# Performance work log

Measured on AMD Instinct MI355X. Metric: run time of the kernel, lower is better.

The kernel has to match this reference:

```python
import jax, jax.numpy as jnp
import numpy as np

N, F_IN, F_OUT = 8192, 512, 256
ALPHA = 0.2  # LeakyReLU negative slope
MASK_FILL = 9e-15  # value used by the original for non-edges (NOT -inf)


def setup_inputs() -> dict:
    key = jax.random.key(0)
    k1, k2, k3, k4 = jax.random.split(key, 4)
    x = jax.random.normal(k1, (N, F_IN), dtype=jnp.float32)
    adj = jax.random.randint(k2, (N, N), 0, 2, dtype=jnp.int32)
    # xavier_uniform-like scale
    wscale = np.sqrt(2.0) * np.sqrt(6.0 / (F_IN + F_OUT))
    ascale = np.sqrt(2.0) * np.sqrt(6.0 / (2 * F_OUT + 1))
    W = jax.random.uniform(k3, (F_IN, F_OUT), jnp.float32, -wscale, wscale)
    a = jax.random.uniform(k4, (2 * F_OUT, 1), jnp.float32, -ascale, ascale)
    return {"x": x, "adj": adj, "W": W, "a": a}


def reference(x, adj, W, a):
    # h: [N, F_OUT]
    h = x @ W
    # score_ij = leakyrelu(cat(h_i, h_j) . a) = leakyrelu(h_i.a1 + h_j.a2)
    a1 = a[:F_OUT, 0]   # [F_OUT]
    a2 = a[F_OUT:, 0]   # [F_OUT]
    f1 = h @ a1         # [N]
    f2 = h @ a2         # [N]
    e = jax.nn.leaky_relu(f1[:, None] + f2[None, :], negative_slope=ALPHA)  # [N, N]
    att = jnp.where(adj > 0, e, jnp.float32(MASK_FILL))
    att = jax.nn.softmax(att, axis=1)
    # dropout is a no-op (p=0.0 / inference)
    h_prime = att @ h   # [N, F_OUT]
    return h_prime
```

## Files before the change

kernel.cpp:

```cpp
#include <hip/hip_runtime.h>
#include <hip/hip_bf16.h>
#include <stdint.h>

#define NN 8192
#define FIN 512
#define FOUT 256
#define ALPHAV 0.2f
#define MASKF 9e-15f
#define L2E 1.44269504088896340736f

typedef __attribute__((ext_vector_type(8))) short bf16x8;
typedef __attribute__((ext_vector_type(16))) float f32x16;

static __device__ __forceinline__ float ex2(float x){
#if __has_builtin(__builtin_amdgcn_exp2f)
  return __builtin_amdgcn_exp2f(x);
#else
  return exp2f(x);
#endif
}
static __device__ __forceinline__ unsigned short f2bf(float f){
  __bf16 b = (__bf16)f;
  return __builtin_bit_cast(unsigned short, b);
}
static __device__ __forceinline__ float bf2f(unsigned short u){
  unsigned int v = ((unsigned int)u) << 16;
  return __builtin_bit_cast(float, v);
}

__global__ __launch_bounds__(256) void k_prep(
    const float* __restrict__ Wm, unsigned short* __restrict__ WtHi,
    unsigned short* __restrict__ WtLo)
{
  __shared__ float ls[16 * 256];
  const int t = threadIdx.x;
  const int S = blockIdx.x;
  const int k0 = S * 16;
  {
    const int kk = t >> 4;
    const int n0 = (t & 15) * 16;
#pragma unroll
    for (int q = 0; q < 4; ++q) {
      float4 v = *(const float4*)(Wm + (size_t)(k0 + kk) * FOUT + n0 + q * 4);
      *(float4*)(&ls[kk * 256 + n0 + q * 4]) = v;
    }
  }
  __syncthreads();
  float v[16];
  unsigned short hh[16], ll[16];
#pragma unroll
  for (int kk = 0; kk < 16; ++kk) {
    v[kk] = ls[kk * 256 + t];
    hh[kk] = f2bf(v[kk]);
    ll[kk] = f2bf(v[kk] - bf2f(hh[kk]));
  }
  unsigned short* oh = WtHi + (size_t)S * 4096 + t * 8;
  unsigned short* ol = WtLo + (size_t)S * 4096 + t * 8;
#pragma unroll
  for (int g = 0; g < 2; ++g) {
    ushort4 a, b, c, d;
    a.x = hh[g*8+0]; a.y = hh[g*8+1]; a.z = hh[g*8+2]; a.w = hh[g*8+3];
    b.x = hh[g*8+4]; b.y = hh[g*8+5]; b.z = hh[g*8+6]; b.w = hh[g*8+7];
    c.x = ll[g*8+0]; c.y = ll[g*8+1]; c.z = ll[g*8+2]; c.w = ll[g*8+3];
    d.x = ll[g*8+4]; d.y = ll[g*8+5]; d.z = ll[g*8+6]; d.w = ll[g*8+7];
    *(ushort4*)(oh + g * 2048)     = a;
    *(ushort4*)(oh + g * 2048 + 4) = b;
    *(ushort4*)(ol + g * 2048)     = c;
    *(ushort4*)(ol + g * 2048 + 4) = d;
  }
}

__global__ __launch_bounds__(256, 1) void k_gemm_h(
    const float* __restrict__ x, const unsigned short* __restrict__ WtHi,
    const unsigned short* __restrict__ WtLo, const float* __restrict__ aG,
    unsigned short* __restrict__ hTt, float* __restrict__ f1,
    float* __restrict__ f2)
{
  __shared__ __align__(16) unsigned short xhi[16384];
  __shared__ __align__(16) unsigned short xlo[16384];
  __shared__ __align__(16) unsigned short wsh[3][4096];
  __shared__ __align__(16) unsigned short wsl[3][4096];
  __shared__ __align__(16) float as2[512];
  __shared__ float f1red[4][32], f2red[4][32];

  const int t  = threadIdx.x;
  const int wv = t >> 6;
  const int l  = t & 63;
  const int lh = l >> 5;
  const int lm = l & 31;
  const int i0 = blockIdx.x * 32;

  if (t < 128) {
    float4 v = *(const float4*)(aG + t * 4);
    *(float4*)(&as2[t * 4]) = v;
  }
  {
    const int xi = t >> 3;
    const int kb = (t & 7) * 4;
    const float* xrow = x + (size_t)(i0 + xi) * FIN;
    const int kgb = (t & 7) >> 1;
    const int bo  = (t & 1) * 4;
#pragma unroll
    for (int q = 0; q < 16; ++q) {
      float4 v = *(const float4*)(xrow + kb + q * 32);
      ushort4 h4, l4;
      h4.x = f2bf(v.x); l4.x = f2bf(v.x - bf2f(h4.x));
      h4.y = f2bf(v.y); l4.y = f2bf(v.y - bf2f(h4.y));
      h4.z = f2bf(v.z); l4.z = f2bf(v.z - bf2f(h4.z));
      h4.w = f2bf(v.w); l4.w = f2bf(v.w - bf2f(h4.w));
      const int idx = (q * 4 + kgb) * 256 + xi * 8 + bo;
      *(ushort4*)(&xhi[idx]) = h4;
      *(ushort4*)(&xlo[idx]) = l4;
    }
  }

  f32x16 acc0, acc1;
#pragma unroll
  for (int e = 0; e < 16; ++e) { acc0[e] = 0.f; acc1[e] = 0.f; }

#define SB0 __builtin_amdgcn_sched_barrier(0)
#define WSTAGE(B, S)                                                          \
  do {                                                                        \
    const unsigned short* gh_ = WtHi + (size_t)(S) * 4096 + t * 8;            \
    const unsigned short* gl_ = WtLo + (size_t)(S) * 4096 + t * 8;            \
    __builtin_amdgcn_global_load_lds(                                         \
        (const __attribute__((address_space(1))) unsigned int*)gh_,           \
        (__attribute__((address_space(3))) unsigned int*)(&wsh[B][t * 8]), 16, 0, 0); \
    __builtin_amdgcn_global_load_lds(                                         \
        (const __attribute__((address_space(1))) unsigned int*)(gh_ + 2048),  \
        (__attribute__((address_space(3))) unsigned int*)(&wsh[B][2048 + t * 8]), 16, 0, 0); \
    __builtin_amdgcn_global_load_lds(                                         \
        (const __attribute__((address_space(1))) unsigned int*)gl_,           \
        (__attribute__((address_space(3))) unsigned int*)(&wsl[B][t * 8]), 16, 0, 0); \
    __builtin_amdgcn_global_load_lds(                                         \
        (const __attribute__((address_space(1))) unsigned int*)(gl_ + 2048),  \
        (__attribute__((address_space(3))) unsigned int*)(&wsl[B][2048 + t * 8]), 16, 0, 0); \
  } while (0)

#define GTS(S, BUF, DOISSUE, NBUF, VMC)                                       \
  do {                                                                        \
    asm volatile("s_waitcnt vmcnt(" #VMC ")" ::: "memory");                   \
    __builtin_amdgcn_s_barrier();                                             \
    SB0;                                                                      \
    if (DOISSUE) WSTAGE(NBUF, (S) + 2);                                       \
    SB0;                                                                      \
    const int kgb_ = ((S) * 2 + lh) * 512 + lm * 16;                          \
    bf16x8 bh_ = *(const bf16x8*)(((const char*)xhi) + kgb_);                 \
    bf16x8 bl_ = *(const bf16x8*)(((const char*)xlo) + kgb_);                 \
    const int na_ = lh * 4096 + (wv * 64 + lm) * 16;                          \
    bf16x8 ah0_ = *(const bf16x8*)(((const char*)&wsh[BUF][0]) + na_);        \
    bf16x8 al0_ = *(const bf16x8*)(((const char*)&wsl[BUF][0]) + na_);        \
    bf16x8 ah1_ = *(const bf16x8*)(((const char*)&wsh[BUF][0]) + na_ + 512);  \
    bf16x8 al1_ = *(const bf16x8*)(((const char*)&wsl[BUF][0]) + na_ + 512);  \
    acc0 = __builtin_amdgcn_mfma_f32_32x32x16_bf16(ah0_, bh_, acc0, 0, 0, 0); \
    acc1 = __builtin_amdgcn_mfma_f32_32x32x16_bf16(ah1_, bh_, acc1, 0, 0, 0); \
    acc0 = __builtin_amdgcn_mfma_f32_32x32x16_bf16(ah0_, bl_, acc0, 0, 0, 0); \
    acc1 = __builtin_amdgcn_mfma_f32_32x32x16_bf16(ah1_, bl_, acc1, 0, 0, 0); \
    acc0 = __builtin_amdgcn_mfma_f32_32x32x16_bf16(al0_, bh_, acc0, 0, 0, 0); \
    acc1 = __builtin_amdgcn_mfma_f32_32x32x16_bf16(al1_, bh_, acc1, 0, 0, 0); \
  } while (0)

  asm volatile("s_waitcnt vmcnt(0)" ::: "memory");
  SB0;
  WSTAGE(0, 0);
  SB0;
  WSTAGE(1, 1);
  asm volatile("s_waitcnt lgkmcnt(0)" ::: "memory");
  SB0;

#pragma unroll 1
  for (int p = 0; p < 10; ++p) {
    const int s0 = p * 3;
    GTS(s0 + 0, 0, 1, 2, 4);
    GTS(s0 + 1, 1, 1, 0, 4);
    GTS(s0 + 2, 2, 1, 1, 4);
  }
  GTS(30, 0, 0, 2, 4);
  GTS(31, 1, 0, 0, 0);
#undef SB0
#undef WSTAGE
#undef GTS

  float p1 = 0.f, p2 = 0.f;
#pragma unroll
  for (int reg = 0; reg < 16; ++reg) {
    const int nl = (reg & 3) + 8 * (reg >> 2) + 4 * lh;
    p1 += acc0[reg] * as2[wv * 64 + nl]       + acc1[reg] * as2[wv * 64 + 32 + nl];
    p2 += acc0[reg] * as2[256 + wv * 64 + nl] + acc1[reg] * as2[256 + wv * 64 + 32 + nl];
  }
  p1 += __shfl_xor(p1, 32);
  p2 += __shfl_xor(p2, 32);
  if (l < 32) { f1red[wv][l] = p1; f2red[wv][l] = p2; }
  __syncthreads();
  if (t < 32) {
    f1[i0 + t] = f1red[0][t] + f1red[1][t] + f1red[2][t] + f1red[3][t];
    f2[i0 + t] = f2red[0][t] + f2red[1][t] + f2red[2][t] + f2red[3][t];
  }

  const size_t hb = (size_t)(i0 >> 5) * 8192 + (size_t)(lm >> 3) * 2048 + (lm & 7);
#pragma unroll
  for (int reg = 0; reg < 16; ++reg) {
    const int nl = (reg & 3) + 8 * (reg >> 2) + 4 * lh;
    hTt[hb + (size_t)(wv * 64 + nl) * 8]      = f2bf(acc0[reg]);
    hTt[hb + (size_t)(wv * 64 + 32 + nl) * 8] = f2bf(acc1[reg]);
  }
}

__global__ __launch_bounds__(1024) void k_bound(
    const float* __restrict__ f1, const float* __restrict__ f2,
    float* __restrict__ mhat)
{
  __shared__ float red[16];
  const int t = threadIdx.x;
  float m = -3.0e38f;
#pragma unroll
  for (int k = 0; k < 8; ++k) m = fmaxf(m, f2[t + k * 1024]);
#pragma unroll
  for (int off = 32; off > 0; off >>= 1) m = fmaxf(m, __shfl_xor(m, off));
  if ((t & 63) == 0) red[t >> 6] = m;
  __syncthreads();
  float fm = red[0];
#pragma unroll
  for (int w = 1; w < 16; ++w) fm = fmaxf(fm, red[w]);
#pragma unroll
  for (int k = 0; k < 8; ++k) {
    int i = t + k * 1024;
    float s = f1[i] + fm;
    mhat[i] = fmaxf(fmaxf(s, ALPHAV * s), MASKF);
  }
}

__global__ __launch_bounds__(256, 2) void k_spmm(
    const unsigned short* __restrict__ hTt,
    const int* __restrict__ adj,
    const float* __restrict__ f1, const float* __restrict__ f2,
    const float* __restrict__ mhat,
    float* __restrict__ part, float* __restrict__ rowsumP)
{
  __shared__ __align__(16) unsigned short hbuf[3 * 8192];
  __shared__ __align__(16) unsigned int mskL[32 * 129];
  __shared__ __align__(16) float f2s[1024];
  const int t  = threadIdx.x;
  const int wv = t >> 6;
  const int l  = t & 63;
  const int lh = l >> 5;
  const int lm = l & 31;
  const int bx = blockIdx.x;
  const int ks = blockIdx.y;
  const int r0 = bx * 128;
  const int lh8 = lh * 8;

  const int rA = r0 + wv * 32 + lm;
  const float nmA   = -mhat[rA] * L2E;
  const float base0 = fmaf(f1[rA], L2E, nmA);
  const float c20   = nmA * (1.f - ALPHAV);
  const float mc0   = fmaf(MASKF, L2E, nmA);

  {
    float4 v = *(const float4*)(f2 + ks * 1024 + t * 4);
    v.x *= L2E; v.y *= L2E; v.z *= L2E; v.w *= L2E;
    *(float4*)(&f2s[t * 4]) = v;
  }

  {
    const int jt = t & 31;
    const int r8 = t >> 5;
    const int* gp = adj + (size_t)(r0 + r8) * NN + ks * 1024 + jt * 32;
#pragma unroll 2
    for (int p = 0; p < 16; ++p) {
      const int* rp = gp + (size_t)p * 8 * NN;
      int4 v[8];
#pragma unroll
      for (int c = 0; c < 8; ++c) v[c] = *(const int4*)(rp + c * 4);
      unsigned int m = 0;
#pragma unroll
      for (int c = 0; c < 8; ++c) {
        m |= (v[c].x > 0 ? 1u : 0u) << (c * 4 + 0);
        m |= (v[c].y > 0 ? 1u : 0u) << (c * 4 + 1);
        m |= (v[c].z > 0 ? 1u : 0u) << (c * 4 + 2);
        m |= (v[c].w > 0 ? 1u : 0u) << (c * 4 + 3);
      }
      mskL[jt * 129 + p * 8 + r8] = m;
    }
  }
  __builtin_amdgcn_sched_barrier(0);

  f32x16 acc[8];
#pragma unroll
  for (int c = 0; c < 8; ++c)
#pragma unroll
    for (int e = 0; e < 16; ++e) acc[c][e] = 0.f;
  float sumP = 0.f;

  const unsigned short* gt0 = hTt + (size_t)ks * 32 * 8192;
  const char* cbase = (const char*)hbuf;
  const int mrow = wv * 32 + lm;

#define SB0 __builtin_amdgcn_sched_barrier(0)
#define STAGE(BUFI, JT)                                                       \
  do {                                                                        \
    const unsigned short* gp_ = gt0 + (size_t)(JT) * 8192 + t * 8;            \
    char* lp_ = ((char*)hbuf) + (BUFI) * 16384 + t * 16;                      \
    _Pragma("unroll")                                                         \
    for (int c = 0; c < 4; ++c) {                                             \
      __builtin_amdgcn_global_load_lds(                                       \
          (const __attribute__((address_space(1))) unsigned int*)(gp_ + c * 2048), \
          (__attribute__((address_space(3))) unsigned int*)(lp_ + c * 4096),  \
          16, 0, 0);                                                          \
    }                                                                         \
  } while (0)

#define REGEN8(AFR, MB, FB)                                                   \
  do {                                                                        \
    float4 fx_ = *(const float4*)(&f2s[FB]);                                  \
    float4 fy_ = *(const float4*)(&f2s[(FB) + 4]);                            \
    float fv_[8] = {fx_.x, fx_.y, fx_.z, fx_.w, fy_.x, fy_.y, fy_.z, fy_.w};  \
    _Pragma("unroll")                                                         \
    for (int b = 0; b < 8; ++b) {                                             \
      float u_ = base0 + fv_[b];                                              \
      float w_ = fmaxf(u_, fmaf(ALPHAV, u_, c20));                            \
      w_ = (((MB) >> b) & 1u) ? w_ : mc0;                                     \
      float p_ = ex2(w_);                                                     \
      sumP += p_;                                                             \
      AFR[b] = (short)f2bf(p_);                                               \
    }                                                                         \
  } while (0)

#define TS(JT, BUF, NBUF, DOISSUE, VMC)                                       \
  do {                                                                        \
    asm volatile("s_waitcnt vmcnt(" #VMC ")" ::: "memory");                   \
    __builtin_amdgcn_s_barrier();                                             \
    SB0;                                                                      \
    if (DOISSUE) STAGE(NBUF, (JT) + 2);                                       \
    SB0;                                                                      \
    const unsigned int m_ = mskL[(JT) * 129 + mrow];                          \
    bf16x8 afr0_, afr1_;                                                      \
    REGEN8(afr0_, m_ >> lh8,        (JT) * 32 + lh8);                         \
    REGEN8(afr1_, m_ >> (16 + lh8), (JT) * 32 + 16 + lh8);                    \
    SB0;                                                                      \
    const char* lb_ = cbase + (BUF) * 16384;                                  \
    const int g0_ = lh * 4096;                                                \
    const int g1_ = (2 + lh) * 4096;                                          \
    const int cb_ = lm * 16;                                                  \
    _Pragma("unroll")                                                         \
    for (int c = 0; c < 8; ++c) {                                             \
      bf16x8 b0_ = *(const bf16x8*)(lb_ + g0_ + c * 512 + cb_);               \
      acc[c] = __builtin_amdgcn_mfma_f32_32x32x16_bf16(afr0_, b0_, acc[c], 0, 0, 0); \
      bf16x8 b1_ = *(const bf16x8*)(lb_ + g1_ + c * 512 + cb_);               \
      acc[c] = __builtin_amdgcn_mfma_f32_32x32x16_bf16(afr1_, b1_, acc[c], 0, 0, 0); \
    }                                                                         \
  } while (0)

  STAGE(0, 0);
  SB0;
  STAGE(1, 1);
  asm volatile("s_waitcnt lgkmcnt(0)" ::: "memory");
  SB0;

#pragma unroll 1
  for (int p = 0; p < 10; ++p) {
    const int s0 = p * 3;
    TS(s0 + 0, 0, 2, 1, 4);
    TS(s0 + 1, 1, 0, 1, 4);
    TS(s0 + 2, 2, 1, 1, 4);
  }
  TS(30, 0, 2, 0, 4);
  TS(31, 1, 0, 0, 0);

#undef SB0
#undef STAGE
#undef REGEN8
#undef TS

  sumP += __shfl_xor(sumP, 32);
  if (lh == 0) rowsumP[(size_t)ks * NN + rA] = sumP;

  float* dst = part + (size_t)ks * NN * FOUT;
  const int rowb = r0 + wv * 32 + 4 * lh;
#pragma unroll
  for (int c = 0; c < 8; ++c) {
    const int col = c * 32 + lm;
#pragma unroll
    for (int reg = 0; reg < 16; ++reg) {
      int row = rowb + (reg & 3) + 8 * (reg >> 2);
      dst[(size_t)row * FOUT + col] = acc[c][reg];
    }
  }
}

__global__ __launch_bounds__(256) void k_fin(
    float* __restrict__ outp, const float* __restrict__ part,
    const float* __restrict__ rowsumP)
{
  const int idx4 = blockIdx.x * 256 + threadIdx.x;
  const size_t e = (size_t)idx4 * 4;
  const int i = (int)(e >> 8);
  float rs = 0.f;
#pragma unroll
  for (int p = 0; p < 8; ++p) rs += rowsumP[(size_t)p * NN + i];
  float4 o = {0.f, 0.f, 0.f, 0.f};
#pragma unroll
  for (int p = 0; p < 8; ++p) {
    float4 pv = *(const float4*)(part + (size_t)p * NN * FOUT + e);
    o.x += pv.x; o.y += pv.y; o.z += pv.z; o.w += pv.w;
  }
  float inv = 1.f / rs;
  o.x *= inv; o.y *= inv; o.z *= inv; o.w *= inv;
  *(float4*)(outp + e) = o;
}

extern "C" void kernel_launch(void* const* d_in, const int* in_sizes, int n_in,
                              void* d_out, int out_size, void* d_ws, size_t ws_size,
                              hipStream_t stream)
{
  const float* x  = (const float*)d_in[0];
  const int* adj  = (const int*)d_in[1];
  const float* Wm = (const float*)d_in[2];
  const float* aG = (const float*)d_in[3];
  float* outp = (float*)d_out;

  char* w = (char*)d_ws;
  unsigned short* hTt  = (unsigned short*)(w + 0);
  float* f1            = (float*)(w + 4194304);
  float* f2            = (float*)(w + 4227072);
  float* mhat          = (float*)(w + 4259840);
  float* rowsumP       = (float*)(w + 4292608);
  unsigned short* WtHi = (unsigned short*)(w + 4554752);
  unsigned short* WtLo = (unsigned short*)(w + 4816896);
  float* part          = (float*)(w + 5079040);

  hipLaunchKernelGGL(k_prep,   dim3(32),    dim3(256),  0, stream, Wm, WtHi, WtLo);
  hipLaunchKernelGGL(k_gemm_h, dim3(256),   dim3(256),  0, stream, x, WtHi, WtLo, aG, hTt, f1, f2);
  hipLaunchKernelGGL(k_bound,  dim3(1),     dim3(1024), 0, stream, f1, f2, mhat);
  hipLaunchKernelGGL(k_spmm,   dim3(64, 8), dim3(256),  0, stream, hTt, adj, f1, f2, mhat, part, rowsumP);
  hipLaunchKernelGGL(k_fin,    dim3(2048),  dim3(256),  0, stream, outp, part, rowsumP);
}
```

Baseline: 137.8 us.

## Stream adjacency mask loads through the main loop instead of a prologue

```diff
diff --git a/kernel.cpp b/kernel.cpp
--- a/kernel.cpp
+++ b/kernel.cpp
@@ -238,7 +238,7 @@
     float* __restrict__ part, float* __restrict__ rowsumP)
 {
   __shared__ __align__(16) unsigned short hbuf[3 * 8192];
-  __shared__ __align__(16) unsigned int mskL[32 * 129];
+  __shared__ __align__(16) unsigned int mskR[4][128];
   __shared__ __align__(16) float f2s[1024];
   const int t  = threadIdx.x;
   const int wv = t >> 6;
@@ -256,50 +256,42 @@
   const float c20   = nmA * (1.f - ALPHAV);
   const float mc0   = fmaf(MASKF, L2E, nmA);
 
+  const int* aQ = adj + (size_t)(r0 + (t >> 1)) * NN + ks * 1024 + (t & 1) * 16;
+
   {
     float4 v = *(const float4*)(f2 + ks * 1024 + t * 4);
     v.x *= L2E; v.y *= L2E; v.z *= L2E; v.w *= L2E;
     *(float4*)(&f2s[t * 4]) = v;
   }
 
-  {
-    const int jt = t & 31;
-    const int r8 = t >> 5;
-    const int* gp = adj + (size_t)(r0 + r8) * NN + ks * 1024 + jt * 32;
-#pragma unroll 2
-    for (int p = 0; p < 16; ++p) {
-      const int* rp = gp + (size_t)p * 8 * NN;
-      int4 v[8];
-#pragma unroll
-      for (int c = 0; c < 8; ++c) v[c] = *(const int4*)(rp + c * 4);
-      unsigned int m = 0;
-#pragma unroll
-      for (int c = 0; c < 8; ++c) {
-        m |= (v[c].x > 0 ? 1u : 0u) << (c * 4 + 0);
-        m |= (v[c].y > 0 ? 1u : 0u) << (c * 4 + 1);
-        m |= (v[c].z > 0 ? 1u : 0u) << (c * 4 + 2);
-        m |= (v[c].w > 0 ? 1u : 0u) << (c * 4 + 3);
-      }
-      mskL[jt * 129 + p * 8 + r8] = m;
-    }
-  }
-  __builtin_amdgcn_sched_barrier(0);
-
-  f32x16 acc[8];
-#pragma unroll
-  for (int c = 0; c < 8; ++c)
-#pragma unroll
-    for (int e = 0; e < 16; ++e) acc[c][e] = 0.f;
-  float sumP = 0.f;
-
-  const unsigned short* gt0 = hTt + (size_t)ks * 32 * 8192;
-  const char* cbase = (const char*)hbuf;
-  const int mrow = wv * 32 + lm;
-
 #define SB0 __builtin_amdgcn_sched_barrier(0)
+#define CONV(R0, R1, R2, R3, SLOT)                                            \
+  do {                                                                        \
+    unsigned int mb_ = 0;                                                     \
+    mb_ |= (R0.x > 0 ? 1u : 0u) << 0;  mb_ |= (R0.y > 0 ? 1u : 0u) << 1;      \
+    mb_ |= (R0.z > 0 ? 1u : 0u) << 2;  mb_ |= (R0.w > 0 ? 1u : 0u) << 3;      \
+    mb_ |= (R1.x > 0 ? 1u : 0u) << 4;  mb_ |= (R1.y > 0 ? 1u : 0u) << 5;      \
+    mb_ |= (R1.z > 0 ? 1u : 0u) << 6;  mb_ |= (R1.w > 0 ? 1u : 0u) << 7;      \
+    mb_ |= (R2.x > 0 ? 1u : 0u) << 8;  mb_ |= (R2.y > 0 ? 1u : 0u) << 9;      \
+    mb_ |= (R2.z > 0 ? 1u : 0u) << 10; mb_ |= (R2.w > 0 ? 1u : 0u) << 11;     \
+    mb_ |= (R3.x > 0 ? 1u : 0u) << 12; mb_ |= (R3.y > 0 ? 1u : 0u) << 13;     \
+    mb_ |= (R3.z > 0 ? 1u : 0u) << 14; mb_ |= (R3.w > 0 ? 1u : 0u) << 15;     \
+    unsigned int ob_ = __shfl_xor(mb_, 1);                                    \
+    if (!(t & 1)) mskR[SLOT][t >> 1] = mb_ | (ob_ << 16);                     \
+  } while (0)
+
+#define ADJR(R0, R1, R2, R3, W)                                               \
+  do {                                                                        \
+    R0 = *(const int4*)(aQ + (W) * 32);                                       \
+    R1 = *(const int4*)(aQ + (W) * 32 + 4);                                   \
+    R2 = *(const int4*)(aQ + (W) * 32 + 8);                                   \
+    R3 = *(const int4*)(aQ + (W) * 32 + 12);                                  \
+  } while (0)
+
 #define STAGE(BUFI, JT)                                                       \
   do {                                                                        \
-    const unsigned short* gp_ = gt0 + (size_t)(JT) * 8192 + t * 8;            \
+    const unsigned short* gp_ = hTt + (size_t)ks * 32 * 8192                  \
+                                + (size_t)(JT) * 8192 + t * 8;                \
     char* lp_ = ((char*)hbuf) + (BUFI) * 16384 + t * 16;                      \
     _Pragma("unroll")                                                         \
     for (int c = 0; c < 4; ++c) {                                             \
@@ -326,14 +318,16 @@
     }                                                                         \
   } while (0)
 
-#define TS(JT, BUF, NBUF, DOISSUE, VMC)                                       \
+#define TS(JT, BUF, NBUF, R0, R1, R2, R3, DOCONV, DOSTAGE, DOADJ, VMC)        \
   do {                                                                        \
     asm volatile("s_waitcnt vmcnt(" #VMC ")" ::: "memory");                   \
     __builtin_amdgcn_s_barrier();                                             \
     SB0;                                                                      \
-    if (DOISSUE) STAGE(NBUF, (JT) + 2);                                       \
+    if (DOCONV) CONV(R0, R1, R2, R3, ((JT) + 2) & 3);                         \
+    if (DOSTAGE) STAGE(NBUF, (JT) + 2);                                       \
+    if (DOADJ) ADJR(R0, R1, R2, R3, (JT) + 4);                                \
     SB0;                                                                      \
-    const unsigned int m_ = mskL[(JT) * 129 + mrow];                          \
+    const unsigned int m_ = mskR[(JT) & 3][mrow];                             \
     bf16x8 afr0_, afr1_;                                                      \
     REGEN8(afr0_, m_ >> lh8,        (JT) * 32 + lh8);                         \
     REGEN8(afr1_, m_ >> (16 + lh8), (JT) * 32 + 16 + lh8);                    \
@@ -351,23 +345,58 @@
     }                                                                         \
   } while (0)
 
+  {
+    int4 a0 = *(const int4*)(aQ + 0),  a1 = *(const int4*)(aQ + 4);
+    int4 a2 = *(const int4*)(aQ + 8),  a3 = *(const int4*)(aQ + 12);
+    CONV(a0, a1, a2, a3, 0);
+    int4 b0 = *(const int4*)(aQ + 32), b1 = *(const int4*)(aQ + 36);
+    int4 b2 = *(const int4*)(aQ + 40), b3 = *(const int4*)(aQ + 44);
+    CONV(b0, b1, b2, b3, 1);
+  }
+  SB0;
+
+  f32x16 acc[8];
+#pragma unroll
+  for (int c = 0; c < 8; ++c)
+#pragma unroll
+    for (int e = 0; e < 16; ++e) acc[c][e] = 0.f;
+  float sumP = 0.f;
+
+  const char* cbase = (const char*)hbuf;
+  const int mrow = wv * 32 + lm;
+
+  int4 X0, X1, X2, X3, Y0, Y1, Y2, Y3;
+
   STAGE(0, 0);
+  ADJR(X0, X1, X2, X3, 2);
   SB0;
   STAGE(1, 1);
+  ADJR(Y0, Y1, Y2, Y3, 3);
   asm volatile("s_waitcnt lgkmcnt(0)" ::: "memory");
   SB0;
 
 #pragma unroll 1
-  for (int p = 0; p < 10; ++p) {
-    const int s0 = p * 3;
-    TS(s0 + 0, 0, 2, 1, 4);
-    TS(s0 + 1, 1, 0, 1, 4);
-    TS(s0 + 2, 2, 1, 1, 4);
-  }
-  TS(30, 0, 2, 0, 4);
-  TS(31, 1, 0, 0, 0);
+  for (int p = 0; p < 4; ++p) {
+    const int s0 = p * 6;
+    TS(s0 + 0, 0, 2, X0, X1, X2, X3, 1, 1, 1, 8);
+    TS(s0 + 1, 1, 0, Y0, Y1, Y2, Y3, 1, 1, 1, 8);
+    TS(s0 + 2, 2, 1, X0, X1, X2, X3, 1, 1, 1, 8);
+    TS(s0 + 3, 0, 2, Y0, Y1, Y2, Y3, 1, 1, 1, 8);
+    TS(s0 + 4, 1, 0, X0, X1, X2, X3, 1, 1, 1, 8);
+    TS(s0 + 5, 2, 1, Y0, Y1, Y2, Y3, 1, 1, 1, 8);
+  }
+  TS(24, 0, 2, X0, X1, X2, X3, 1, 1, 1, 8);
+  TS(25, 1, 0, Y0, Y1, Y2, Y3, 1, 1, 1, 8);
+  TS(26, 2, 1, X0, X1, X2, X3, 1, 1, 1, 8);
+  TS(27, 0, 2, Y0, Y1, Y2, Y3, 1, 1, 1, 8);
+  TS(28, 1, 0, X0, X1, X2, X3, 1, 1, 0, 8);
+  TS(29, 2, 1, Y0, Y1, Y2, Y3, 1, 1, 0, 4);
+  TS(30, 0, 2, X0, X1, X2, X3, 0, 0, 0, 4);
+  TS(31, 1, 0, Y0, Y1, Y2, Y3, 0, 0, 0, 0);
 
 #undef SB0
+#undef CONV
+#undef ADJR
 #undef STAGE
 #undef REGEN8
 #undef TS
```

Result: slower. 174.5 us (+26.6%).

## Halve spmm row tile, split waves 2x2 over columns, and prefetch next attention fragment

Applied to the files above, without the earlier changes.

```diff
diff --git a/kernel.cpp b/kernel.cpp
--- a/kernel.cpp
+++ b/kernel.cpp
@@ -238,19 +238,21 @@
     float* __restrict__ part, float* __restrict__ rowsumP)
 {
   __shared__ __align__(16) unsigned short hbuf[3 * 8192];
-  __shared__ __align__(16) unsigned int mskL[32 * 129];
+  __shared__ __align__(16) unsigned int mskL[32 * 66];
   __shared__ __align__(16) float f2s[1024];
   const int t  = threadIdx.x;
   const int wv = t >> 6;
   const int l  = t & 63;
   const int lh = l >> 5;
   const int lm = l & 31;
+  const int wr = wv >> 1;
+  const int wc = wv & 1;
   const int bx = blockIdx.x;
   const int ks = blockIdx.y;
-  const int r0 = bx * 128;
+  const int r0 = bx * 64;
   const int lh8 = lh * 8;
 
-  const int rA = r0 + wv * 32 + lm;
+  const int rA = r0 + wr * 32 + lm;
   const float nmA   = -mhat[rA] * L2E;
   const float base0 = fmaf(f1[rA], L2E, nmA);
   const float c20   = nmA * (1.f - ALPHAV);
@@ -267,7 +269,7 @@
     const int r8 = t >> 5;
     const int* gp = adj + (size_t)(r0 + r8) * NN + ks * 1024 + jt * 32;
 #pragma unroll 2
-    for (int p = 0; p < 16; ++p) {
+    for (int p = 0; p < 8; ++p) {
       const int* rp = gp + (size_t)p * 8 * NN;
       int4 v[8];
 #pragma unroll
@@ -280,26 +282,28 @@
         m |= (v[c].z > 0 ? 1u : 0u) << (c * 4 + 2);
         m |= (v[c].w > 0 ? 1u : 0u) << (c * 4 + 3);
       }
-      mskL[jt * 129 + p * 8 + r8] = m;
+      mskL[jt * 66 + p * 8 + r8] = m;
     }
   }
+  asm volatile("s_waitcnt lgkmcnt(0)" ::: "memory");
+  __builtin_amdgcn_s_barrier();
   __builtin_amdgcn_sched_barrier(0);
 
-  f32x16 acc[8];
-#pragma unroll
-  for (int c = 0; c < 8; ++c)
+  f32x16 acc[4];
+#pragma unroll
+  for (int c = 0; c < 4; ++c)
 #pragma unroll
     for (int e = 0; e < 16; ++e) acc[c][e] = 0.f;
   float sumP = 0.f;
 
-  const unsigned short* gt0 = hTt + (size_t)ks * 32 * 8192;
   const char* cbase = (const char*)hbuf;
-  const int mrow = wv * 32 + lm;
+  const int mrow = wr * 32 + lm;
 
 #define SB0 __builtin_amdgcn_sched_barrier(0)
 #define STAGE(BUFI, JT)                                                       \
   do {                                                                        \
-    const unsigned short* gp_ = gt0 + (size_t)(JT) * 8192 + t * 8;            \
+    const unsigned short* gp_ = hTt + (size_t)ks * 32 * 8192                  \
+                                + (size_t)(JT) * 8192 + t * 8;                \
     char* lp_ = ((char*)hbuf) + (BUFI) * 16384 + t * 16;                      \
     _Pragma("unroll")                                                         \
     for (int c = 0; c < 4; ++c) {                                             \
@@ -326,60 +330,69 @@
     }                                                                         \
   } while (0)
 
-#define TS(JT, BUF, NBUF, DOISSUE, VMC)                                       \
+#define REGEN_STEP(A0, A1, JT)                                                \
+  do {                                                                        \
+    const unsigned int m_ = mskL[(JT) * 66 + mrow];                           \
+    REGEN8(A0, m_ >> lh8,        (JT) * 32 + lh8);                            \
+    REGEN8(A1, m_ >> (16 + lh8), (JT) * 32 + 16 + lh8);                       \
+  } while (0)
+
+#define TS(JT, BUF, NBUF, C0, C1, N0, N1, DOREGEN, DOSTAGE, VMC)              \
   do {                                                                        \
     asm volatile("s_waitcnt vmcnt(" #VMC ")" ::: "memory");                   \
     __builtin_amdgcn_s_barrier();                                             \
     SB0;                                                                      \
-    if (DOISSUE) STAGE(NBUF, (JT) + 2);                                       \
+    if (DOSTAGE) STAGE(NBUF, (JT) + 2);                                       \
     SB0;                                                                      \
-    const unsigned int m_ = mskL[(JT) * 129 + mrow];                          \
-    bf16x8 afr0_, afr1_;                                                      \
-    REGEN8(afr0_, m_ >> lh8,        (JT) * 32 + lh8);                         \
-    REGEN8(afr1_, m_ >> (16 + lh8), (JT) * 32 + 16 + lh8);                    \
-    SB0;                                                                      \
+    if (DOREGEN) REGEN_STEP(N0, N1, (JT) + 1);                                \
     const char* lb_ = cbase + (BUF) * 16384;                                  \
     const int g0_ = lh * 4096;                                                \
     const int g1_ = (2 + lh) * 4096;                                          \
-    const int cb_ = lm * 16;                                                  \
+    const int cb_ = (wc * 128 + lm) * 16;                                     \
     _Pragma("unroll")                                                         \
-    for (int c = 0; c < 8; ++c) {                                             \
+    for (int c = 0; c < 4; ++c) {                                             \
       bf16x8 b0_ = *(const bf16x8*)(lb_ + g0_ + c * 512 + cb_);               \
-      acc[c] = __builtin_amdgcn_mfma_f32_32x32x16_bf16(afr0_, b0_, acc[c], 0, 0, 0); \
+      acc[c] = __builtin_amdgcn_mfma_f32_32x32x16_bf16(C0, b0_, acc[c], 0, 0, 0); \
       bf16x8 b1_ = *(const bf16x8*)(lb_ + g1_ + c * 512 + cb_);               \
-      acc[c] = __builtin_amdgcn_mfma_f32_32x32x16_bf16(afr1_, b1_, acc[c], 0, 0, 0); \
+      acc[c] = __builtin_amdgcn_mfma_f32_32x32x16_bf16(C1, b1_, acc[c], 0, 0, 0); \
     }                                                                         \
   } while (0)
 
+  bf16x8 aE0, aE1, aO0, aO1;
+  REGEN_STEP(aE0, aE1, 0);
+  SB0;
   STAGE(0, 0);
   SB0;
   STAGE(1, 1);
-  asm volatile("s_waitcnt lgkmcnt(0)" ::: "memory");
   SB0;
 
 #pragma unroll 1
-  for (int p = 0; p < 10; ++p) {
-    const int s0 = p * 3;
-    TS(s0 + 0, 0, 2, 1, 4);
-    TS(s0 + 1, 1, 0, 1, 4);
-    TS(s0 + 2, 2, 1, 1, 4);
-  }
-  TS(30, 0, 2, 0, 4);
-  TS(31, 1, 0, 0, 0);
+  for (int p = 0; p < 5; ++p) {
+    const int s0 = p * 6;
+    TS(s0 + 0, 0, 2, aE0, aE1, aO0, aO1, 1, 1, 4);
+    TS(s0 + 1, 1, 0, aO0, aO1, aE0, aE1, 1, 1, 4);
+    TS(s0 + 2, 2, 1, aE0, aE1, aO0, aO1, 1, 1, 4);
+    TS(s0 + 3, 0, 2, aO0, aO1, aE0, aE1, 1, 1, 4);
+    TS(s0 + 4, 1, 0, aE0, aE1, aO0, aO1, 1, 1, 4);
+    TS(s0 + 5, 2, 1, aO0, aO1, aE0, aE1, 1, 1, 4);
+  }
+  TS(30, 0, 2, aE0, aE1, aO0, aO1, 1, 0, 4);
+  TS(31, 1, 0, aO0, aO1, aE0, aE1, 0, 0, 0);
 
 #undef SB0
 #undef STAGE
 #undef REGEN8
+#undef REGEN_STEP
 #undef TS
 
   sumP += __shfl_xor(sumP, 32);
-  if (lh == 0) rowsumP[(size_t)ks * NN + rA] = sumP;
+  if (lh == 0 && wc == 0) rowsumP[(size_t)ks * NN + rA] = sumP;
 
   float* dst = part + (size_t)ks * NN * FOUT;
-  const int rowb = r0 + wv * 32 + 4 * lh;
-#pragma unroll
-  for (int c = 0; c < 8; ++c) {
-    const int col = c * 32 + lm;
+  const int rowb = r0 + wr * 32 + 4 * lh;
+#pragma unroll
+  for (int c = 0; c < 4; ++c) {
+    const int col = wc * 128 + c * 32 + lm;
 #pragma unroll
     for (int reg = 0; reg < 16; ++reg) {
       int row = rowb + (reg & 3) + 8 * (reg >> 2);
@@ -429,9 +442,9 @@
   unsigned short* WtLo = (unsigned short*)(w + 4816896);
   float* part          = (float*)(w + 5079040);
 
-  hipLaunchKernelGGL(k_prep,   dim3(32),    dim3(256),  0, stream, Wm, WtHi, WtLo);
-  hipLaunchKernelGGL(k_gemm_h, dim3(256),   dim3(256),  0, stream, x, WtHi, WtLo, aG, hTt, f1, f2);
-  hipLaunchKernelGGL(k_bound,  dim3(1),     dim3(1024), 0, stream, f1, f2, mhat);
-  hipLaunchKernelGGL(k_spmm,   dim3(64, 8), dim3(256),  0, stream, hTt, adj, f1, f2, mhat, part, rowsumP);
-  hipLaunchKernelGGL(k_fin,    dim3(2048),  dim3(256),  0, stream, outp, part, rowsumP);
-}
+  hipLaunchKernelGGL(k_prep,   dim3(32),     dim3(256),  0, stream, Wm, WtHi, WtLo);
+  hipLaunchKernelGGL(k_gemm_h, dim3(256),    dim3(256),  0, stream, x, WtHi, WtLo, aG, hTt, f1, f2);
+  hipLaunchKernelGGL(k_bound,  dim3(1),      dim3(1024), 0, stream, f1, f2, mhat);
+  hipLaunchKernelGGL(k_spmm,   dim3(128, 8), dim3(256),  0, stream, hTt, adj, f1, f2, mhat, part, rowsumP);
+  hipLaunchKernelGGL(k_fin,    dim3(2048),   dim3(256),  0, stream, outp, part, rowsumP);
+}
```

New measurement: 151.2 us. 9.7% more time.

## Stream adjacency mask loads into MFMA loop and store bf16 partials

Applied to the files above, without the earlier changes.

```diff
diff --git a/kernel.cpp b/kernel.cpp
--- a/kernel.cpp
+++ b/kernel.cpp
@@ -235,10 +235,10 @@
     const int* __restrict__ adj,
     const float* __restrict__ f1, const float* __restrict__ f2,
     const float* __restrict__ mhat,
-    float* __restrict__ part, float* __restrict__ rowsumP)
+    unsigned short* __restrict__ partB, float* __restrict__ rowsumP)
 {
   __shared__ __align__(16) unsigned short hbuf[3 * 8192];
-  __shared__ __align__(16) unsigned int mskL[32 * 129];
+  __shared__ __align__(16) unsigned int mskD[2][8][128];
   __shared__ __align__(16) float f2s[1024];
   const int t  = threadIdx.x;
   const int wv = t >> 6;
@@ -249,6 +249,8 @@
   const int ks = blockIdx.y;
   const int r0 = bx * 128;
   const int lh8 = lh * 8;
+  const int arow = t >> 3;
+  const int awrd = t & 7;
 
   const int rA = r0 + wv * 32 + lm;
   const float nmA   = -mhat[rA] * L2E;
@@ -262,44 +264,45 @@
     *(float4*)(&f2s[t * 4]) = v;
   }
 
-  {
-    const int jt = t & 31;
-    const int r8 = t >> 5;
-    const int* gp = adj + (size_t)(r0 + r8) * NN + ks * 1024 + jt * 32;
-#pragma unroll 2
-    for (int p = 0; p < 16; ++p) {
-      const int* rp = gp + (size_t)p * 8 * NN;
-      int4 v[8];
-#pragma unroll
-      for (int c = 0; c < 8; ++c) v[c] = *(const int4*)(rp + c * 4);
-      unsigned int m = 0;
-#pragma unroll
-      for (int c = 0; c < 8; ++c) {
-        m |= (v[c].x > 0 ? 1u : 0u) << (c * 4 + 0);
-        m |= (v[c].y > 0 ? 1u : 0u) << (c * 4 + 1);
-        m |= (v[c].z > 0 ? 1u : 0u) << (c * 4 + 2);
-        m |= (v[c].w > 0 ? 1u : 0u) << (c * 4 + 3);
-      }
-      mskL[jt * 129 + p * 8 + r8] = m;
-    }
-  }
-  __builtin_amdgcn_sched_barrier(0);
-
-  f32x16 acc[8];
-#pragma unroll
-  for (int c = 0; c < 8; ++c)
-#pragma unroll
-    for (int e = 0; e < 16; ++e) acc[c][e] = 0.f;
-  float sumP = 0.f;
-
-  const unsigned short* gt0 = hTt + (size_t)ks * 32 * 8192;
-  const char* cbase = (const char*)hbuf;
-  const int mrow = wv * 32 + lm;
+  int4 g0, g1, g2, g3, g4, g5, g6, g7;
 
 #define SB0 __builtin_amdgcn_sched_barrier(0)
+#define ADJP(P, CN)                                                           \
+  do {                                                                        \
+    const int* ap_ = adj + (size_t)(r0 + (P) * 32 + arow) * NN                \
+                     + ks * 1024 + (CN) * 256 + awrd * 32;                    \
+    g0 = ((const int4*)ap_)[0]; g1 = ((const int4*)ap_)[1];                   \
+    g2 = ((const int4*)ap_)[2]; g3 = ((const int4*)ap_)[3];                   \
+    g4 = ((const int4*)ap_)[4]; g5 = ((const int4*)ap_)[5];                   \
+    g6 = ((const int4*)ap_)[6]; g7 = ((const int4*)ap_)[7];                   \
+  } while (0)
+
+#define CONVP(P, PAR)                                                         \
+  do {                                                                        \
+    unsigned int m_ = 0;                                                      \
+    m_ |= (g0.x>0?1u:0u)<<0;  m_ |= (g0.y>0?1u:0u)<<1;                        \
+    m_ |= (g0.z>0?1u:0u)<<2;  m_ |= (g0.w>0?1u:0u)<<3;                        \
+    m_ |= (g1.x>0?1u:0u)<<4;  m_ |= (g1.y>0?1u:0u)<<5;                        \
+    m_ |= (g1.z>0?1u:0u)<<6;  m_ |= (g1.w>0?1u:0u)<<7;                        \
+    m_ |= (g2.x>0?1u:0u)<<8;  m_ |= (g2.y>0?1u:0u)<<9;                        \
+    m_ |= (g2.z>0?1u:0u)<<10; m_ |= (g2.w>0?1u:0u)<<11;                       \
+    m_ |= (g3.x>0?1u:0u)<<12; m_ |= (g3.y>0?1u:0u)<<13;                       \
+    m_ |= (g3.z>0?1u:0u)<<14; m_ |= (g3.w>0?1u:0u)<<15;                       \
+    m_ |= (g4.x>0?1u:0u)<<16; m_ |= (g4.y>0?1u:0u)<<17;                       \
+    m_ |= (g4.z>0?1u:0u)<<18; m_ |= (g4.w>0?1u:0u)<<19;                       \
+    m_ |= (g5.x>0?1u:0u)<<20; m_ |= (g5.y>0?1u:0u)<<21;                       \
+    m_ |= (g5.z>0?1u:0u)<<22; m_ |= (g5.w>0?1u:0u)<<23;                       \
+    m_ |= (g6.x>0?1u:0u)<<24; m_ |= (g6.y>0?1u:0u)<<25;                       \
+    m_ |= (g6.z>0?1u:0u)<<26; m_ |= (g6.w>0?1u:0u)<<27;                       \
+    m_ |= (g7.x>0?1u:0u)<<28; m_ |= (g7.y>0?1u:0u)<<29;                       \
+    m_ |= (g7.z>0?1u:0u)<<30; m_ |= (g7.w>0?1u:0u)<<31;                       \
+    mskD[PAR][awrd][(P) * 32 + arow] = m_;                                    \
+  } while (0)
+
 #define STAGE(BUFI, JT)                                                       \
   do {                                                                        \
-    const unsigned short* gp_ = gt0 + (size_t)(JT) * 8192 + t * 8;            \
+    const unsigned short* gp_ = hTt + (size_t)ks * 32 * 8192                  \
+                                + (size_t)(JT) * 8192 + t * 8;                \
     char* lp_ = ((char*)hbuf) + (BUFI) * 16384 + t * 16;                      \
     _Pragma("unroll")                                                         \
     for (int c = 0; c < 4; ++c) {                                             \
@@ -326,56 +329,104 @@
     }                                                                         \
   } while (0)
 
-#define TS(JT, BUF, NBUF, DOISSUE, VMC)                                       \
+#define STEP(JT, BUF, NBUF, DOSTAGE, VMC, DOCONV, CP, CPAR, DOADJ, AP, ACN)   \
   do {                                                                        \
     asm volatile("s_waitcnt vmcnt(" #VMC ")" ::: "memory");                   \
     __builtin_amdgcn_s_barrier();                                             \
     SB0;                                                                      \
-    if (DOISSUE) STAGE(NBUF, (JT) + 2);                                       \
-    SB0;                                                                      \
-    const unsigned int m_ = mskL[(JT) * 129 + mrow];                          \
+    if (DOCONV) CONVP(CP, CPAR);                                              \
+    if (DOSTAGE) STAGE(NBUF, (JT) + 2);                                       \
+    SB0;                                                                      \
+    if (DOADJ) ADJP(AP, ACN);                                                 \
+    SB0;                                                                      \
+    const unsigned int m_ = mskD[((JT) >> 3) & 1][(JT) & 7][mrow];            \
     bf16x8 afr0_, afr1_;                                                      \
     REGEN8(afr0_, m_ >> lh8,        (JT) * 32 + lh8);                         \
     REGEN8(afr1_, m_ >> (16 + lh8), (JT) * 32 + 16 + lh8);                    \
     SB0;                                                                      \
     const char* lb_ = cbase + (BUF) * 16384;                                  \
-    const int g0_ = lh * 4096;                                                \
-    const int g1_ = (2 + lh) * 4096;                                          \
+    const int gg0_ = lh * 4096;                                               \
+    const int gg1_ = (2 + lh) * 4096;                                         \
     const int cb_ = lm * 16;                                                  \
     _Pragma("unroll")                                                         \
     for (int c = 0; c < 8; ++c) {                                             \
-      bf16x8 b0_ = *(const bf16x8*)(lb_ + g0_ + c * 512 + cb_);               \
+      bf16x8 b0_ = *(const bf16x8*)(lb_ + gg0_ + c * 512 + cb_);              \
       acc[c] = __builtin_amdgcn_mfma_f32_32x32x16_bf16(afr0_, b0_, acc[c], 0, 0, 0); \
-      bf16x8 b1_ = *(const bf16x8*)(lb_ + g1_ + c * 512 + cb_);               \
+      bf16x8 b1_ = *(const bf16x8*)(lb_ + gg1_ + c * 512 + cb_);              \
       acc[c] = __builtin_amdgcn_mfma_f32_32x32x16_bf16(afr1_, b1_, acc[c], 0, 0, 0); \
     }                                                                         \
   } while (0)
 
+#pragma unroll
+  for (int p = 0; p < 4; ++p) {
+    ADJP(p, 0);
+    CONVP(p, 0);
+  }
+  asm volatile("s_waitcnt lgkmcnt(0)" ::: "memory");
+  __builtin_amdgcn_s_barrier();
+  SB0;
+
+  f32x16 acc[8];
+#pragma unroll
+  for (int c = 0; c < 8; ++c)
+#pragma unroll
+    for (int e = 0; e < 16; ++e) acc[c][e] = 0.f;
+  float sumP = 0.f;
+
+  const char* cbase = (const char*)hbuf;
+  const int mrow = wv * 32 + lm;
+
+  asm volatile("s_waitcnt vmcnt(0)" ::: "memory");
+  SB0;
   STAGE(0, 0);
   SB0;
   STAGE(1, 1);
-  asm volatile("s_waitcnt lgkmcnt(0)" ::: "memory");
-  SB0;
-
-#pragma unroll 1
-  for (int p = 0; p < 10; ++p) {
-    const int s0 = p * 3;
-    TS(s0 + 0, 0, 2, 1, 4);
-    TS(s0 + 1, 1, 0, 1, 4);
-    TS(s0 + 2, 2, 1, 1, 4);
-  }
-  TS(30, 0, 2, 0, 4);
-  TS(31, 1, 0, 0, 0);
+  SB0;
+
+  STEP(0, 0, 2, 1, 4,  0, 0, 0, 1, 0, 1);
+  STEP(1, 1, 0, 1, 12, 1, 0, 1, 1, 1, 1);
+  STEP(2, 2, 1, 1, 20, 1, 1, 1, 1, 2, 1);
+  STEP(3, 0, 2, 1, 20, 1, 2, 1, 1, 3, 1);
+  STEP(4, 1, 0, 1, 20, 1, 3, 1, 0, 0, 0);
+  STEP(5, 2, 1, 1, 12, 0, 0, 0, 0, 0, 0);
+  STEP(6, 0, 2, 1, 4,  0, 0, 0, 0, 0, 0);
+  STEP(7, 1, 0, 1, 4,  0, 0, 0, 0, 0, 0);
+  STEP(8,  2, 1, 1, 4,  0, 0, 0, 1, 0, 2);
+  STEP(9,  0, 2, 1, 12, 1, 0, 0, 1, 1, 2);
+  STEP(10, 1, 0, 1, 20, 1, 1, 0, 1, 2, 2);
+  STEP(11, 2, 1, 1, 20, 1, 2, 0, 1, 3, 2);
+  STEP(12, 0, 2, 1, 20, 1, 3, 0, 0, 0, 0);
+  STEP(13, 1, 0, 1, 12, 0, 0, 0, 0, 0, 0);
+  STEP(14, 2, 1, 1, 4,  0, 0, 0, 0, 0, 0);
+  STEP(15, 0, 2, 1, 4,  0, 0, 0, 0, 0, 0);
+  STEP(16, 1, 0, 1, 4,  0, 0, 0, 1, 0, 3);
+  STEP(17, 2, 1, 1, 12, 1, 0, 1, 1, 1, 3);
+  STEP(18, 0, 2, 1, 20, 1, 1, 1, 1, 2, 3);
+  STEP(19, 1, 0, 1, 20, 1, 2, 1, 1, 3, 3);
+  STEP(20, 2, 1, 1, 20, 1, 3, 1, 0, 0, 0);
+  STEP(21, 0, 2, 1, 12, 0, 0, 0, 0, 0, 0);
+  STEP(22, 1, 0, 1, 4,  0, 0, 0, 0, 0, 0);
+  STEP(23, 2, 1, 1, 4,  0, 0, 0, 0, 0, 0);
+  STEP(24, 0, 2, 1, 4,  0, 0, 0, 0, 0, 0);
+  STEP(25, 1, 0, 1, 4,  0, 0, 0, 0, 0, 0);
+  STEP(26, 2, 1, 1, 4,  0, 0, 0, 0, 0, 0);
+  STEP(27, 0, 2, 1, 4,  0, 0, 0, 0, 0, 0);
+  STEP(28, 1, 0, 1, 4,  0, 0, 0, 0, 0, 0);
+  STEP(29, 2, 1, 1, 4,  0, 0, 0, 0, 0, 0);
+  STEP(30, 0, 2, 0, 4,  0, 0, 0, 0, 0, 0);
+  STEP(31, 1, 0, 0, 0,  0, 0, 0, 0, 0, 0);
 
 #undef SB0
+#undef ADJP
+#undef CONVP
 #undef STAGE
 #undef REGEN8
-#undef TS
+#undef STEP
 
   sumP += __shfl_xor(sumP, 32);
   if (lh == 0) rowsumP[(size_t)ks * NN + rA] = sumP;
 
-  float* dst = part + (size_t)ks * NN * FOUT;
+  unsigned short* dst = partB + (size_t)ks * NN * FOUT;
   const int rowb = r0 + wv * 32 + 4 * lh;
 #pragma unroll
   for (int c = 0; c < 8; ++c) {
@@ -383,13 +434,13 @@
 #pragma unroll
     for (int reg = 0; reg < 16; ++reg) {
       int row = rowb + (reg & 3) + 8 * (reg >> 2);
-      dst[(size_t)row * FOUT + col] = acc[c][reg];
+      dst[(size_t)row * FOUT + col] = f2bf(acc[c][reg]);
     }
   }
 }
 
 __global__ __launch_bounds__(256) void k_fin(
-    float* __restrict__ outp, const float* __restrict__ part,
+    float* __restrict__ outp, const unsigned short* __restrict__ partB,
     const float* __restrict__ rowsumP)
 {
   const int idx4 = blockIdx.x * 256 + threadIdx.x;
@@ -401,8 +452,9 @@
   float4 o = {0.f, 0.f, 0.f, 0.f};
 #pragma unroll
   for (int p = 0; p < 8; ++p) {
-    float4 pv = *(const float4*)(part + (size_t)p * NN * FOUT + e);
-    o.x += pv.x; o.y += pv.y; o.z += pv.z; o.w += pv.w;
+    ushort4 pv = *(const ushort4*)(partB + (size_t)p * NN * FOUT + e);
+    o.x += bf2f(pv.x); o.y += bf2f(pv.y);
+    o.z += bf2f(pv.z); o.w += bf2f(pv.w);
   }
   float inv = 1.f / rs;
   o.x *= inv; o.y *= inv; o.z *= inv; o.w *= inv;
@@ -427,11 +479,11 @@
   float* rowsumP       = (float*)(w + 4292608);
   unsigned short* WtHi = (unsigned short*)(w + 4554752);
   unsigned short* WtLo = (unsigned short*)(w + 4816896);
-  float* part          = (float*)(w + 5079040);
+  unsigned short* partB= (unsigned short*)(w + 5079040);
 
   hipLaunchKernelGGL(k_prep,   dim3(32),    dim3(256),  0, stream, Wm, WtHi, WtLo);
   hipLaunchKernelGGL(k_gemm_h, dim3(256),   dim3(256),  0, stream, x, WtHi, WtLo, aG, hTt, f1, f2);
   hipLaunchKernelGGL(k_bound,  dim3(1),     dim3(1024), 0, stream, f1, f2, mhat);
-  hipLaunchKernelGGL(k_spmm,   dim3(64, 8), dim3(256),  0, stream, hTt, adj, f1, f2, mhat, part, rowsumP);
-  hipLaunchKernelGGL(k_fin,    dim3(2048),  dim3(256),  0, stream, outp, part, rowsumP);
-}
+  hipLaunchKernelGGL(k_spmm,   dim3(64, 8), dim3(256),  0, stream, hTt, adj, f1, f2, mhat, partB, rowsumP);
+  hipLaunchKernelGGL(k_fin,    dim3(2048),  dim3(256),  0, stream, outp, partB, rowsumP);
+}
```

Result: faster. 128.0 us (-7.1%).
